# Kernel tuning notes

Measured on AMD Instinct MI355X. Metric: run time of the kernel, lower is better.

Reference implementation:

```python
import jax, jax.numpy as jnp
import numpy as np

EPS_LN = 1e-5
EPS_W = 1e-16
K = 3


def layernorm(x, gamma, beta):
    mu = x.mean(-1, keepdims=True)
    var = ((x - mu) ** 2).mean(-1, keepdims=True)
    return (x - mu) * jax.lax.rsqrt(var + EPS_LN) * gamma + beta


def knn_interp(xb, pos_x, pos_y, k=K):
    """Inverse-squared-distance kNN interpolation.
    xb: [B, Nx, C] source features; pos_x: [Nx, 3]; pos_y: [Ny, 3].
    Positions are identical across batch (torch code expands them), so the
    kNN search is done once and the gather is broadcast over batch.
    Returns [B, Ny, C]."""
    # squared distances via ||y||^2 + ||x||^2 - 2 y.x  -> [Ny, Nx]
    d2 = ((pos_y * pos_y).sum(-1)[:, None]
          + (pos_x * pos_x).sum(-1)[None, :]
          - 2.0 * pos_y @ pos_x.T)
    _, idx = jax.lax.top_k(-d2, k)                      # [Ny, k] nearest
    # exact squared distances for the selected neighbors (matches torch math)
    diff = pos_x[idx] - pos_y[:, None, :]               # [Ny, k, 3]
    w = 1.0 / jnp.clip((diff * diff).sum(-1), EPS_W)    # [Ny, k]
    xg = xb[:, idx, :]                                  # [B, Ny, k, C]
    num = (xg * w[None, :, :, None]).sum(2)             # [B, Ny, C]
    return num / w.sum(1)[None, :, None]


def setup_inputs() -> dict:
    key = jax.random.key(0)
    k1, k2, k3 = jax.random.split(key, 3)
    B, N_MESH, N_PIV, C = 4, 40000, 2000, 128
    return {
        "node_features": jax.random.normal(k1, (B * N_MESH, C), jnp.float32),
        "gamma": jnp.ones((C,), jnp.float32),
        "beta": jnp.zeros((C,), jnp.float32),
        "position_mesh": jax.random.uniform(k2, (N_MESH, 3), jnp.float32),
        "position_pivotal": jax.random.uniform(k3, (N_PIV, 3), jnp.float32),
        "batch_size": 4,
    }


def reference(node_features, gamma, beta, position_mesh, position_pivotal, batch_size):
    B = batch_size
    C = node_features.shape[-1]
    Nm = position_mesh.shape[0]
    # encode: PivotalNorm then mesh -> pivotal interpolation
    h = layernorm(node_features, gamma, beta)
    hb = h.reshape(B, Nm, C)
    piv = knn_interp(hb, position_mesh, position_pivotal, K)      # [B, Npiv, C]
    # decode: pivotal -> mesh interpolation
    mesh = knn_interp(piv, position_pivotal, position_mesh, K)    # [B, Nm, C]
    return mesh.reshape(B * Nm, C)
```

## Files before the change

kernel.cpp:

```cpp
#include <hip/hip_runtime.h>
#include <hip/hip_bf16.h>
#include <math.h>

#define EPS_LN 1e-5f
#define EPS_W  1e-16f

__device__ __forceinline__ float cvt(const __hip_bfloat16 v) { return __bfloat162float(v); }
__device__ __forceinline__ float cvt(const float v)          { return v; }

__device__ __forceinline__ void load8(const __hip_bfloat16* p, float* x) {
    union { uint4 v; __hip_bfloat16 h[8]; } t;
    t.v = *(const uint4*)p;
    #pragma unroll
    for (int i = 0; i < 8; ++i) x[i] = __bfloat162float(t.h[i]);
}
__device__ __forceinline__ void load8(const float* p, float* x) {
    float4 a = *(const float4*)p, b = *(const float4*)(p + 4);
    x[0]=a.x; x[1]=a.y; x[2]=a.z; x[3]=a.w; x[4]=b.x; x[5]=b.y; x[6]=b.z; x[7]=b.w;
}

__device__ __forceinline__ void ins3lex(float nd, int ni, float d[3], int ix[3]) {
    bool b2 = (nd < d[2]) || (nd == d[2] && ni < ix[2]);
    if (!b2) return;
    bool b1 = (nd < d[1]) || (nd == d[1] && ni < ix[1]);
    bool b0 = (nd < d[0]) || (nd == d[0] && ni < ix[0]);
    if (b0)      { d[2]=d[1]; ix[2]=ix[1]; d[1]=d[0]; ix[1]=ix[0]; d[0]=nd; ix[0]=ni; }
    else if (b1) { d[2]=d[1]; ix[2]=ix[1]; d[1]=nd; ix[1]=ni; }
    else         { d[2]=nd; ix[2]=ni; }
}

__global__ __launch_bounds__(256)
void stage_kernel(const void* pmesh, int Nm, const void* ppiv, int Np,
                  float4* __restrict__ mesh_s, float4* __restrict__ piv_s,
                  int* __restrict__ flag) {
    __shared__ int sbad;
    if (threadIdx.x == 0) sbad = 0;
    __syncthreads();
    {
        const __hip_bfloat16* pb = (const __hip_bfloat16*)ppiv;
        int bad = 0;
        for (int i = threadIdx.x; i < Np * 3; i += 256) {
            float v = __bfloat162float(pb[i]);
            if (!(v >= 0.0f && v <= 1.0f)) bad = 1;
        }
        if (bad) sbad = 1;
    }
    __syncthreads();
    const int isf32 = sbad;

    int gid = blockIdx.x * 256 + threadIdx.x;
    if (gid == 0) *flag = isf32;
    const int total = Nm + Np;
    if (gid >= total) return;
    const int isMesh = gid < Nm ? 1 : 0;
    const int idx = isMesh ? gid : gid - Nm;
    const void* src = isMesh ? pmesh : ppiv;
    float x, y, z;
    if (isf32) {
        const float* p = (const float*)src;
        x = p[idx*3+0]; y = p[idx*3+1]; z = p[idx*3+2];
    } else {
        const __hip_bfloat16* p = (const __hip_bfloat16*)src;
        x = cvt(p[idx*3+0]); y = cvt(p[idx*3+1]); z = cvt(p[idx*3+2]);
    }
    float4 o; o.x = x; o.y = y; o.z = z; o.w = x*x + y*y + z*z;
    (isMesh ? mesh_s : piv_s)[idx] = o;
}

__device__ __forceinline__ void scan_body(
        const float4* __restrict__ cand, int Nc,
        const float4* __restrict__ qry, int Nq,
        int blk, int nslice, int chunk,
        int* __restrict__ idx_out, float* __restrict__ wn_out,
        float2* __restrict__ partials,
        float sd[4][64][3], int si[4][64][3]) {
    const int tid   = threadIdx.x;
    const int lane  = tid & 63;
    const int wv    = __builtin_amdgcn_readfirstlane(tid >> 6);
    const int qg    = blk / nslice;
    const int slice = blk % nslice;
    const int q     = qg * 64 + lane;
    const int qc    = min(q, Nq - 1);

    const float4 qp = qry[qc];
    const float  qn = qp.w;

    float d0 = INFINITY, d1 = INFINITY, d2 = INFINITY;
    int   i0 = 0x7fffffff, i1 = 0x7fffffff, i2 = 0x7fffffff;

    const int jbeg = (slice * 4 + wv) * chunk;
    const int jend = min(jbeg + chunk, Nc);
    #pragma unroll 4
    for (int j = jbeg; j < jend; ++j) {
        const float4 cp = cand[j];
        float t   = qn + cp.w;
        float dot = qp.x*cp.x + qp.y*cp.y + qp.z*cp.z;
        float s   = t - 2.0f*dot;
        if (__any(s < d2)) {
            if (s < d2) {
                if (s < d1) {
                    d2 = d1; i2 = i1;
                    if (s < d0) { d1 = d0; i1 = i0; d0 = s; i0 = j; }
                    else        { d1 = s;  i1 = j; }
                } else { d2 = s; i2 = j; }
            }
        }
    }

    sd[wv][lane][0] = d0; sd[wv][lane][1] = d1; sd[wv][lane][2] = d2;
    si[wv][lane][0] = i0; si[wv][lane][1] = i1; si[wv][lane][2] = i2;
    __syncthreads();

    if (wv == 0) {
        float d[3]  = {d0, d1, d2};
        int   ix[3] = {i0, i1, i2};
        for (int w = 1; w < 4; ++w)
            for (int k = 0; k < 3; ++k)
                ins3lex(sd[w][lane][k], si[w][lane][k], d, ix);
        if (q < Nq) {
            if (nslice == 1) {
                float w_[3], ws = 0.f;
                for (int k = 0; k < 3; ++k) {
                    int ii = min(max(ix[k], 0), Nc - 1);
                    ix[k] = ii;
                    float4 cp = cand[ii];
                    float dx = cp.x - qp.x, dy = cp.y - qp.y, dz = cp.z - qp.z;
                    float dd = dx*dx + dy*dy + dz*dz;
                    w_[k] = 1.0f / fmaxf(dd, EPS_W);
                    ws += w_[k];
                }
                float inv = 1.0f / ws;
                for (int k = 0; k < 3; ++k) {
                    idx_out[q*3+k] = ix[k];
                    wn_out[q*3+k]  = w_[k] * inv;
                }
            } else {
                float2* p = partials + ((size_t)q * nslice + slice) * 3;
                for (int k = 0; k < 3; ++k) {
                    float2 e; e.x = d[k]; e.y = __int_as_float(ix[k]);
                    p[k] = e;
                }
            }
        }
    }
}

__global__ __launch_bounds__(256)
void knn_scan_fused(const float4* __restrict__ mesh_s, int Nm,
                    const float4* __restrict__ piv_s, int Np,
                    int nb1, int nsl1, int chk1, int nsl2, int chk2,
                    int* __restrict__ idx1, float* __restrict__ wn1,
                    float2* __restrict__ part1,
                    int* __restrict__ idx2, float* __restrict__ wn2,
                    float2* __restrict__ part2) {
    __shared__ float sd[4][64][3];
    __shared__ int   si[4][64][3];
    const int bid = blockIdx.x;
    if (bid < nb1) {
        scan_body(mesh_s, Nm, piv_s, Np, bid, nsl1, chk1,
                  idx1, wn1, part1, sd, si);
    } else {
        scan_body(piv_s, Np, mesh_s, Nm, bid - nb1, nsl2, chk2,
                  idx2, wn2, part2, sd, si);
    }
}

__device__ __forceinline__ void finalize_wave(
        const float2* __restrict__ partials, int nslice,
        const float4* __restrict__ cand, int Nc,
        const float4* __restrict__ qry, int q, int lane,
        int* __restrict__ idx_out, float* __restrict__ wn_out) {
    const int nent = nslice * 3;
    const float2* p = partials + (size_t)q * nent;

    float d[3]  = {INFINITY, INFINITY, INFINITY};
    int   ix[3] = {0x7fffffff, 0x7fffffff, 0x7fffffff};
    for (int e = lane; e < nent; e += 64)
        ins3lex(p[e].x, __float_as_int(p[e].y), d, ix);

    #pragma unroll
    for (int off = 32; off >= 1; off >>= 1) {
        float od[3]; int oix[3];
        #pragma unroll
        for (int k = 0; k < 3; ++k) {
            od[k]  = __shfl_xor(d[k],  off);
            oix[k] = __shfl_xor(ix[k], off);
        }
        #pragma unroll
        for (int k = 0; k < 3; ++k) ins3lex(od[k], oix[k], d, ix);
    }

    if (lane == 0) {
        const float4 qp = qry[q];
        float w_[3], ws = 0.f;
        for (int k = 0; k < 3; ++k) {
            int ii = min(max(ix[k], 0), Nc - 1);
            ix[k] = ii;
            float4 cp = cand[ii];
            float dx = cp.x - qp.x, dy = cp.y - qp.y, dz = cp.z - qp.z;
            float dd = dx*dx + dy*dy + dz*dz;
            w_[k] = 1.0f / fmaxf(dd, EPS_W);
            ws += w_[k];
        }
        float inv = 1.0f / ws;
        for (int k = 0; k < 3; ++k) {
            idx_out[q*3+k] = ix[k];
            wn_out[q*3+k]  = w_[k] * inv;
        }
    }
}

__global__ __launch_bounds__(256)
void knn_finalize_fused(const float2* __restrict__ part1, int nsl1,
                        const float4* __restrict__ mesh_s, int Nm,
                        const float4* __restrict__ piv_s, int Np,
                        const float2* __restrict__ part2, int nsl2,
                        int nq1, int nq2,
                        int* __restrict__ idx1, float* __restrict__ wn1,
                        int* __restrict__ idx2, float* __restrict__ wn2) {
    const int lane = threadIdx.x & 63;
    const int w = blockIdx.x * 4 + (threadIdx.x >> 6);
    if (w < nq1)
        finalize_wave(part1, nsl1, mesh_s, Nm, piv_s, w, lane, idx1, wn1);
    else if (w - nq1 < nq2)
        finalize_wave(part2, nsl2, piv_s, Np, mesh_s, w - nq1, lane, idx2, wn2);
}

template <typename T, typename S>
__device__ void interp_ln_wave4_body(const T* __restrict__ xfeat,
                                     const T* __restrict__ gamma,
                                     const T* __restrict__ beta,
                                     const int* __restrict__ idx,
                                     const float* __restrict__ wn,
                                     S* __restrict__ piv,
                                     int Nm, int Np, int C, int B) {
    const int tid  = threadIdx.x;
    const int lane = tid & 63;
    const int sub  = lane >> 4;
    const int l16  = lane & 15;
    const int row_id = (blockIdx.x * 4 + (tid >> 6)) * 4 + sub;
    if (row_id >= B * Np) return;
    const int b  = row_id / Np;
    const int j  = row_id - b * Np;
    const int c0 = l16 * 8;

    float g[8], be[8];
    load8(gamma + c0, g);
    load8(beta  + c0, be);

    const float invC = 1.0f / (float)C;
    float acc[8];
    #pragma unroll
    for (int t = 0; t < 8; ++t) acc[t] = 0.f;

    for (int k = 0; k < 3; ++k) {
        int row = idx[j*3+k];
        row = min(max(row, 0), Nm - 1);
        const T* xp = xfeat + ((size_t)b*Nm + row) * (size_t)C + c0;
        float x[8];
        load8(xp, x);
        float s = 0.f, s2 = 0.f;
        #pragma unroll
        for (int t = 0; t < 8; ++t) { s += x[t]; s2 += x[t]*x[t]; }
        #pragma unroll
        for (int off = 8; off >= 1; off >>= 1) {
            s  += __shfl_xor(s,  off);
            s2 += __shfl_xor(s2, off);
        }
        float mean = s * invC;
        float var  = s2 * invC - mean*mean;
        float rs   = rsqrtf(var + EPS_LN);
        float wk   = wn[j*3+k];
        #pragma unroll
        for (int t = 0; t < 8; ++t)
            acc[t] += wk * ((x[t] - mean)*rs*g[t] + be[t]);
    }

    S* pp = piv + ((size_t)b*Np + j) * (size_t)C + c0;
    if constexpr (sizeof(S) == 2) {
        union { uint4 v; S h[8]; } o;
        #pragma unroll
        for (int t = 0; t < 8; ++t) o.h[t] = __float2bfloat16(acc[t]);
        *(uint4*)pp = o.v;
    } else {
        float4 a, c;
        a.x = acc[0]; a.y = acc[1]; a.z = acc[2]; a.w = acc[3];
        c.x = acc[4]; c.y = acc[5]; c.z = acc[6]; c.w = acc[7];
        *(float4*)pp = a;
        *(float4*)(pp + 4) = c;
    }
}

__global__ __launch_bounds__(256)
void interp_ln_wave4_kernel(const void* xfeat, const void* gamma, const void* beta,
                            const int* idx, const float* wn, void* piv,
                            int Nm, int Np, int C, int B, const int* dtype_flag) {
    if (*dtype_flag)
        interp_ln_wave4_body<float, float>((const float*)xfeat, (const float*)gamma,
                                           (const float*)beta, idx, wn,
                                           (float*)piv, Nm, Np, C, B);
    else
        interp_ln_wave4_body<__hip_bfloat16, __hip_bfloat16>(
            (const __hip_bfloat16*)xfeat, (const __hip_bfloat16*)gamma,
            (const __hip_bfloat16*)beta, idx, wn,
            (__hip_bfloat16*)piv, Nm, Np, C, B);
}

template <typename T, typename S>
__device__ void interp_ln_body(const T* __restrict__ xfeat,
                               const T* __restrict__ gamma,
                               const T* __restrict__ beta,
                               const int* __restrict__ idx,
                               const float* __restrict__ wn,
                               S* __restrict__ piv, int Nm, int Np, int C) {
    const int j   = blockIdx.x % Np;
    const int b   = blockIdx.x / Np;
    const int c   = threadIdx.x;
    const int wid = c >> 6;
    const int nw  = C >> 6;

    const float g  = cvt(gamma[c]);
    const float be = cvt(beta[c]);

    __shared__ float red[8];
    float acc = 0.f;
    const float invC = 1.0f / (float)C;

    for (int k = 0; k < 3; ++k) {
        int row = idx[j*3+k];
        row = min(max(row, 0), Nm - 1);
        const T* xp = xfeat + ((size_t)b*Nm + row) * (size_t)C;
        float x = cvt(xp[c]);
        float s = x, s2 = x*x;
        for (int off = 32; off > 0; off >>= 1) {
            s  += __shfl_down(s,  off);
            s2 += __shfl_down(s2, off);
        }
        if ((c & 63) == 0) { red[wid] = s; red[4+wid] = s2; }
        __syncthreads();
        float sum = 0.f, sum2 = 0.f;
        for (int w = 0; w < nw; ++w) { sum += red[w]; sum2 += red[4+w]; }
        float mean = sum * invC;
        float var  = sum2 * invC - mean*mean;
        float rs   = rsqrtf(var + EPS_LN);
        acc += wn[j*3+k] * ((x - mean)*rs*g + be);
        __syncthreads();
    }
    S ov; if constexpr (sizeof(S) == 2) ov = __float2bfloat16(acc); else ov = acc;
    piv[((size_t)b*Np + j) * (size_t)C + c] = ov;
}

__global__ __launch_bounds__(128)
void interp_ln_kernel(const void* xfeat, const void* gamma, const void* beta,
                      const int* idx, const float* wn, void* piv,
                      int Nm, int Np, int C, const int* dtype_flag) {
    if (*dtype_flag)
        interp_ln_body<float, float>((const float*)xfeat, (const float*)gamma,
                                     (const float*)beta, idx, wn,
                                     (float*)piv, Nm, Np, C);
    else
        interp_ln_body<__hip_bfloat16, __hip_bfloat16>(
            (const __hip_bfloat16*)xfeat, (const __hip_bfloat16*)gamma,
            (const __hip_bfloat16*)beta, idx, wn,
            (__hip_bfloat16*)piv, Nm, Np, C);
}

__global__ __launch_bounds__(256)
void gather_out8_kernel(const void* __restrict__ pivv,
                        const int* __restrict__ idx, const float* __restrict__ wn,
                        void* __restrict__ out, int Nm, int Np, int C, int B,
                        int total, const int* __restrict__ dtype_flag) {
    int gid = blockIdx.x * 256 + threadIdx.x;
    if (gid >= total) return;
    const int C8 = C >> 3;
    const int c8 = gid % C8;
    const int i  = gid / C8;
    int jj0 = min(max(idx[i*3+0], 0), Np - 1);
    int jj1 = min(max(idx[i*3+1], 0), Np - 1);
    int jj2 = min(max(idx[i*3+2], 0), Np - 1);
    const float w0 = wn[i*3+0], w1 = wn[i*3+1], w2 = wn[i*3+2];
    const int cb = c8 * 8;

    if (*dtype_flag) {
        const float* pv = (const float*)pivv;
        float* po = (float*)out;
        for (int b = 0; b < B; ++b) {
            const float* pb = pv + (size_t)b * Np * C;
            const float* r0 = pb + (size_t)jj0 * C + cb;
            const float* r1 = pb + (size_t)jj1 * C + cb;
            const float* r2 = pb + (size_t)jj2 * C + cb;
            float* qo = po + ((size_t)b*Nm + i) * (size_t)C + cb;
            #pragma unroll
            for (int h = 0; h < 2; ++h) {
                float4 v0 = *(const float4*)(r0 + h*4);
                float4 v1 = *(const float4*)(r1 + h*4);
                float4 v2 = *(const float4*)(r2 + h*4);
                float4 o;
                o.x = w0*v0.x + w1*v1.x + w2*v2.x;
                o.y = w0*v0.y + w1*v1.y + w2*v2.y;
                o.z = w0*v0.z + w1*v1.z + w2*v2.z;
                o.w = w0*v0.w + w1*v1.w + w2*v2.w;
                *(float4*)(qo + h*4) = o;
            }
        }
    } else {
        const __hip_bfloat16* pv = (const __hip_bfloat16*)pivv;
        __hip_bfloat16* po = (__hip_bfloat16*)out;
        for (int b = 0; b < B; ++b) {
            const __hip_bfloat16* pb = pv + (size_t)b * Np * C;
            union { uint4 v; __hip_bfloat16 h[8]; } u0, u1, u2, o;
            u0.v = *(const uint4*)(pb + (size_t)jj0 * C + cb);
            u1.v = *(const uint4*)(pb + (size_t)jj1 * C + cb);
            u2.v = *(const uint4*)(pb + (size_t)jj2 * C + cb);
            #pragma unroll
            for (int t = 0; t < 8; ++t) {
                float a = w0*cvt(u0.h[t]) + w1*cvt(u1.h[t]) + w2*cvt(u2.h[t]);
                o.h[t] = __float2bfloat16(a);
            }
            *(uint4*)(po + ((size_t)b*Nm + i) * (size_t)C + cb) = o.v;
        }
    }
}

__global__ __launch_bounds__(256)
void gather_out_kernel(const void* __restrict__ pivv,
                       const int* __restrict__ idx, const float* __restrict__ wn,
                       void* __restrict__ out, int Nm, int Np, int C4,
                       int total4, const int* __restrict__ dtype_flag) {
    int gid = blockIdx.x * 256 + threadIdx.x;
    if (gid >= total4) return;
    int c4 = gid % C4;
    int r  = gid / C4;
    int i  = r % Nm;
    int b  = r / Nm;
    const int C = C4 * 4;
    int jj0 = min(max(idx[i*3+0], 0), Np - 1);
    int jj1 = min(max(idx[i*3+1], 0), Np - 1);
    int jj2 = min(max(idx[i*3+2], 0), Np - 1);
    float w0 = wn[i*3+0], w1 = wn[i*3+1], w2 = wn[i*3+2];

    if (*dtype_flag) {
        const float* pbase = (const float*)pivv + (size_t)b * Np * C;
        float4 v0 = *(const float4*)(pbase + (size_t)jj0 * C + c4*4);
        float4 v1 = *(const float4*)(pbase + (size_t)jj1 * C + c4*4);
        float4 v2 = *(const float4*)(pbase + (size_t)jj2 * C + c4*4);
        float4 o;
        o.x = w0*v0.x + w1*v1.x + w2*v2.x;
        o.y = w0*v0.y + w1*v1.y + w2*v2.y;
        o.z = w0*v0.z + w1*v1.z + w2*v2.z;
        o.w = w0*v0.w + w1*v1.w + w2*v2.w;
        *(((float4*)out) + gid) = o;
    } else {
        const __hip_bfloat16* pbase = (const __hip_bfloat16*)pivv + (size_t)b * Np * C;
        union { __hip_bfloat16 h[4]; uint2 v; } u0, u1, u2, o;
        u0.v = *(const uint2*)(pbase + (size_t)jj0 * C + c4*4);
        u1.v = *(const uint2*)(pbase + (size_t)jj1 * C + c4*4);
        u2.v = *(const uint2*)(pbase + (size_t)jj2 * C + c4*4);
        #pragma unroll
        for (int t = 0; t < 4; ++t) {
            float a = w0*cvt(u0.h[t]) + w1*cvt(u1.h[t]) + w2*cvt(u2.h[t]);
            o.h[t] = __float2bfloat16(a);
        }
        *(((uint2*)out) + gid) = o.v;
    }
}

__global__ void zero_words_kernel(unsigned* out, long long nwords) {
    long long i = (long long)blockIdx.x * 256 + threadIdx.x;
    if (i < nwords) out[i] = 0u;
}

extern "C" void kernel_launch(void* const* d_in, const int* in_sizes, int n_in,
                              void* d_out, int out_size, void* d_ws, size_t ws_size,
                              hipStream_t stream) {
    const int C  = in_sizes[1];
    const int Nm = in_sizes[3] / 3;
    const int Np = in_sizes[4] / 3;
    const int B  = in_sizes[0] / (Nm * C);

    const int nqg1 = (Np + 63) / 64;
    const int nqg2 = (Nm + 63) / 64;

    auto plan = [](int nqg, int Nc, int& nsl, int& chk) {
        nsl = (2048 + nqg - 1) / nqg;
        int maxsl = (Nc + 127) / 128;
        if (nsl > maxsl) nsl = maxsl;
        if (nsl < 1) nsl = 1;
        chk = (Nc + nsl*4 - 1) / (nsl*4);
    };
    int nsl1, chk1, nsl2, chk2;
    plan(nqg1, Nm, nsl1, chk1);
    plan(nqg2, Np, nsl2, chk2);

    size_t off = 0;
    size_t flag_o = 0, meshs_o = 0, pivs_o = 0, piv_o = 0;
    size_t i1_o = 0, w1_o = 0, i2_o = 0, w2_o = 0, p1_o = 0, p2_o = 0;
    auto layout = [&](int s1, int s2) {
        off = 0;
        auto carve = [&](size_t bytes) {
            size_t p = off;
            off += (bytes + 255) & ~(size_t)255;
            return p;
        };
        flag_o  = carve(256);
        meshs_o = carve((size_t)Nm * sizeof(float4));
        pivs_o  = carve((size_t)Np * sizeof(float4));
        piv_o   = carve((size_t)B * Np * C * sizeof(float));
        i1_o    = carve((size_t)Np * 3 * sizeof(int));
        w1_o    = carve((size_t)Np * 3 * sizeof(float));
        i2_o    = carve((size_t)Nm * 3 * sizeof(int));
        w2_o    = carve((size_t)Nm * 3 * sizeof(float));
        p1_o    = carve((size_t)Np * s1 * 3 * sizeof(float2));
        p2_o    = carve((size_t)Nm * s2 * 3 * sizeof(float2));
    };
    layout(nsl1, nsl2);
    if (off > ws_size) {
        nsl1 = 16; chk1 = (Nm + nsl1*4 - 1) / (nsl1*4);
        nsl2 = 1;  chk2 = (Np + nsl2*4 - 1) / (nsl2*4);
        layout(nsl1, nsl2);
    }
    if (off > ws_size) {
        long long nwords = (long long)out_size / 2;
        zero_words_kernel<<<(int)((nwords + 255) / 256), 256, 0, stream>>>(
            (unsigned*)d_out, nwords);
        return;
    }

    char* base = (char*)d_ws;
    int*    flag   = (int*)   (base + flag_o);
    float4* mesh_s = (float4*)(base + meshs_o);
    float4* piv_s  = (float4*)(base + pivs_o);
    void*   piv    = (void*)  (base + piv_o);
    int*    idx1   = (int*)   (base + i1_o);
    float*  wn1    = (float*) (base + w1_o);
    int*    idx2   = (int*)   (base + i2_o);
    float*  wn2    = (float*) (base + w2_o);
    float2* part1  = (float2*)(base + p1_o);
    float2* part2  = (float2*)(base + p2_o);

    stage_kernel<<<(Nm + Np + 255) / 256, 256, 0, stream>>>(
        d_in[3], Nm, d_in[4], Np, mesh_s, piv_s, flag);

    const int nb1 = nqg1 * nsl1;
    const int nb2 = nqg2 * nsl2;
    knn_scan_fused<<<nb1 + nb2, 256, 0, stream>>>(
        mesh_s, Nm, piv_s, Np, nb1, nsl1, chk1, nsl2, chk2,
        idx1, wn1, part1, idx2, wn2, part2);

    const int nq1 = (nsl1 > 1) ? Np : 0;
    const int nq2 = (nsl2 > 1) ? Nm : 0;
    if (nq1 + nq2 > 0)
        knn_finalize_fused<<<(nq1 + nq2 + 3) / 4, 256, 0, stream>>>(
            part1, nsl1, mesh_s, Nm, piv_s, Np, part2, nsl2,
            nq1, nq2, idx1, wn1, idx2, wn2);

    if (C == 128) {
        const int nrow = B * Np;
        interp_ln_wave4_kernel<<<(nrow + 15) / 16, 256, 0, stream>>>(
            d_in[0], d_in[1], d_in[2], idx1, wn1, piv, Nm, Np, C, B, flag);
    } else {
        interp_ln_kernel<<<B * Np, C, 0, stream>>>(d_in[0], d_in[1], d_in[2],
                                                   idx1, wn1, piv, Nm, Np, C, flag);
    }

    if ((C & 7) == 0) {
        const int total = Nm * (C >> 3);
        gather_out8_kernel<<<(total + 255) / 256, 256, 0, stream>>>(
            piv, idx2, wn2, d_out, Nm, Np, C, B, total, flag);
    } else {
        const int C4 = C / 4;
        const int total4 = B * Nm * C4;
        gather_out_kernel<<<(total4 + 255) / 256, 256, 0, stream>>>(
            piv, idx2, wn2, d_out, Nm, Np, C4, total4, flag);
    }
}
```

Measured before the change: 265.0 us.

## Use uniform grid spatial binning for mesh-to-pivotal kNN search

Replaces the brute-force scan of all 40k mesh points per pivotal query with a uniform 3D grid: points are counted per cell, prefix-summed, and scattered into cell order. Each wave then searches growing shells of cells around its query and stops once the shell distance bound exceeds the current third-nearest distance. A brute-force fallback runs when mesh positions fall outside the unit cube. It also drops the wave-level __any guard in the remaining brute-force scan. The cost is four extra small launches (zero, count, single-block scan, scatter), atomics, and divergent shell loops, in exchange for far fewer distance evaluations.

```diff
diff --git a/kernel.cpp b/kernel.cpp
--- a/kernel.cpp
+++ b/kernel.cpp
@@ -4,6 +4,8 @@
 
 #define EPS_LN 1e-5f
 #define EPS_W  1e-16f
+#define SLACK_KNN 1e-4f
+#define IMAX 0x7fffffff
 
 __device__ __forceinline__ float cvt(const __hip_bfloat16 v) { return __bfloat162float(v); }
 __device__ __forceinline__ float cvt(const float v)          { return v; }
@@ -29,10 +31,24 @@
     else         { d[2]=nd; ix[2]=ni; }
 }
 
+__device__ __forceinline__ void wave_merge3(float d[3], int ix[3]) {
+    #pragma unroll
+    for (int off = 32; off >= 1; off >>= 1) {
+        float od[3]; int oix[3];
+        #pragma unroll
+        for (int k = 0; k < 3; ++k) {
+            od[k]  = __shfl_xor(d[k],  off);
+            oix[k] = __shfl_xor(ix[k], off);
+        }
+        #pragma unroll
+        for (int k = 0; k < 3; ++k) ins3lex(od[k], oix[k], d, ix);
+    }
+}
+
 __global__ __launch_bounds__(256)
 void stage_kernel(const void* pmesh, int Nm, const void* ppiv, int Np,
                   float4* __restrict__ mesh_s, float4* __restrict__ piv_s,
-                  int* __restrict__ flag) {
+                  int* __restrict__ flag, int* __restrict__ counts, int G1) {
     __shared__ int sbad;
     if (threadIdx.x == 0) sbad = 0;
     __syncthreads();
@@ -49,7 +65,7 @@
     const int isf32 = sbad;
 
     int gid = blockIdx.x * 256 + threadIdx.x;
-    if (gid == 0) *flag = isf32;
+    if (gid == 0) flag[0] = isf32;
     const int total = Nm + Np;
     if (gid >= total) return;
     const int isMesh = gid < Nm ? 1 : 0;
@@ -65,6 +81,63 @@
     }
     float4 o; o.x = x; o.y = y; o.z = z; o.w = x*x + y*y + z*z;
     (isMesh ? mesh_s : piv_s)[idx] = o;
+
+    if (isMesh) {
+        int cx = min(max((int)(x * (float)G1), 0), G1 - 1);
+        int cy = min(max((int)(y * (float)G1), 0), G1 - 1);
+        int cz = min(max((int)(z * (float)G1), 0), G1 - 1);
+        atomicAdd(&counts[(cz * G1 + cy) * G1 + cx], 1);
+        bool ok = (x >= 0.f && x <= 1.f && y >= 0.f && y <= 1.f &&
+                   z >= 0.f && z <= 1.f);
+        if (!ok) atomicOr(&flag[1], 1);
+    }
+}
+
+__global__ __launch_bounds__(256)
+void scan_kernel(const int* __restrict__ counts, int n,
+                 int* __restrict__ starts, int* __restrict__ cursors) {
+    __shared__ int carry;
+    __shared__ int wsum[4];
+    if (threadIdx.x == 0) carry = 0;
+    __syncthreads();
+    const int lane = threadIdx.x & 63;
+    const int wv   = threadIdx.x >> 6;
+    for (int base = 0; base < n; base += 256) {
+        int i = base + threadIdx.x;
+        int v = (i < n) ? counts[i] : 0;
+        int s = v;
+        #pragma unroll
+        for (int off = 1; off < 64; off <<= 1) {
+            int t = __shfl_up(s, off);
+            if (lane >= off) s += t;
+        }
+        if (lane == 63) wsum[wv] = s;
+        __syncthreads();
+        int woff = 0;
+        for (int w = 0; w < wv; ++w) woff += wsum[w];
+        int excl = carry + woff + (s - v);
+        if (i < n) { starts[i] = excl; cursors[i] = excl; }
+        __syncthreads();
+        if (threadIdx.x == 255) carry += woff + s;
+        __syncthreads();
+    }
+    if (threadIdx.x == 0) starts[n] = carry;
+}
+
+__global__ __launch_bounds__(256)
+void scatter_kernel(const float4* __restrict__ mesh_s, int Nm, int G1,
+                    int* __restrict__ cursors,
+                    float4* __restrict__ cellPts, int* __restrict__ cellIdx) {
+    int gid = blockIdx.x * 256 + threadIdx.x;
+    if (gid >= Nm) return;
+    float4 p = mesh_s[gid];
+    int cx = min(max((int)(p.x * (float)G1), 0), G1 - 1);
+    int cy = min(max((int)(p.y * (float)G1), 0), G1 - 1);
+    int cz = min(max((int)(p.z * (float)G1), 0), G1 - 1);
+    int c = (cz * G1 + cy) * G1 + cx;
+    int pos = atomicAdd(&cursors[c], 1);
+    cellPts[pos] = p;
+    cellIdx[pos] = gid;
 }
 
 __device__ __forceinline__ void scan_body(
@@ -86,7 +159,7 @@
     const float  qn = qp.w;
 
     float d0 = INFINITY, d1 = INFINITY, d2 = INFINITY;
-    int   i0 = 0x7fffffff, i1 = 0x7fffffff, i2 = 0x7fffffff;
+    int   i0 = IMAX, i1 = IMAX, i2 = IMAX;
 
     const int jbeg = (slice * 4 + wv) * chunk;
     const int jend = min(jbeg + chunk, Nc);
@@ -96,14 +169,12 @@
         float t   = qn + cp.w;
         float dot = qp.x*cp.x + qp.y*cp.y + qp.z*cp.z;
         float s   = t - 2.0f*dot;
-        if (__any(s < d2)) {
-            if (s < d2) {
-                if (s < d1) {
-                    d2 = d1; i2 = i1;
-                    if (s < d0) { d1 = d0; i1 = i0; d0 = s; i0 = j; }
-                    else        { d1 = s;  i1 = j; }
-                } else { d2 = s; i2 = j; }
-            }
+        if (s < d2) {
+            if (s < d1) {
+                d2 = d1; i2 = i1;
+                if (s < d0) { d1 = d0; i1 = i0; d0 = s; i0 = j; }
+                else        { d1 = s;  i1 = j; }
+            } else { d2 = s; i2 = j; }
         }
     }
 
@@ -146,49 +217,160 @@
 }
 
 __global__ __launch_bounds__(256)
-void knn_scan_fused(const float4* __restrict__ mesh_s, int Nm,
-                    const float4* __restrict__ piv_s, int Np,
-                    int nb1, int nsl1, int chk1, int nsl2, int chk2,
-                    int* __restrict__ idx1, float* __restrict__ wn1,
-                    float2* __restrict__ part1,
-                    int* __restrict__ idx2, float* __restrict__ wn2,
-                    float2* __restrict__ part2) {
+void knn_fused(const float4* __restrict__ mesh_s, int Nm,
+               const float4* __restrict__ piv_s, int Np,
+               const int* __restrict__ starts,
+               const float4* __restrict__ cellPts,
+               const int* __restrict__ cellIdx,
+               int G1, int nbW, int nsl2, int chk2,
+               int* __restrict__ idx1, float* __restrict__ wn1,
+               int* __restrict__ idx2, float* __restrict__ wn2,
+               float2* __restrict__ part2,
+               const int* __restrict__ flags) {
     __shared__ float sd[4][64][3];
     __shared__ int   si[4][64][3];
     const int bid = blockIdx.x;
-    if (bid < nb1) {
-        scan_body(mesh_s, Nm, piv_s, Np, bid, nsl1, chk1,
-                  idx1, wn1, part1, sd, si);
+
+    if (bid >= nbW) {
+        scan_body(piv_s, Np, mesh_s, Nm, bid - nbW, nsl2, chk2,
+                  idx2, wn2, part2, sd, si);
+        return;
+    }
+
+    const int lane = threadIdx.x & 63;
+    const int wv   = threadIdx.x >> 6;
+    const int q    = bid * 4 + wv;
+    if (q >= Np) return;
+
+    const float4 qp = piv_s[q];
+    const float  qn = qp.w;
+    float d[3]  = {INFINITY, INFINITY, INFINITY};
+    int   ix[3] = {IMAX, IMAX, IMAX};
+
+    if (!flags[1]) {
+        const float Gf = (float)G1;
+        const float h  = 1.0f / Gf;
+        int cx = min(max((int)(qp.x * Gf), 0), G1 - 1);
+        int cy = min(max((int)(qp.y * Gf), 0), G1 - 1);
+        int cz = min(max((int)(qp.z * Gf), 0), G1 - 1);
+        cx = __builtin_amdgcn_readfirstlane(cx);
+        cy = __builtin_amdgcn_readfirstlane(cy);
+        cz = __builtin_amdgcn_readfirstlane(cz);
+        float fx0 = qp.x - (float)cx * h,  fx1 = (float)(cx+1) * h - qp.x;
+        float fy0 = qp.y - (float)cy * h,  fy1 = (float)(cy+1) * h - qp.y;
+        float fz0 = qp.z - (float)cz * h,  fz1 = (float)(cz+1) * h - qp.z;
+        float fmin = fminf(fminf(fminf(fx0, fx1), fminf(fy0, fy1)),
+                           fminf(fz0, fz1));
+
+        for (int r = 0; r <= G1; ++r) {
+            if (r >= 2) {
+                float md[3] = {d[0], d[1], d[2]};
+                int   mi[3] = {ix[0], ix[1], ix[2]};
+                wave_merge3(md, mi);
+                if (mi[2] != IMAX) {
+                    float bound = (float)(r - 1) * h + fmin;
+                    if (bound > 0.f && bound * bound - SLACK_KNN > md[2])
+                        break;
+                }
+            }
+            for (int dz = -r; dz <= r; ++dz) {
+                int z = cz + dz; if (z < 0 || z >= G1) continue;
+                int adz = dz < 0 ? -dz : dz;
+                for (int dy = -r; dy <= r; ++dy) {
+                    int y = cy + dy; if (y < 0 || y >= G1) continue;
+                    int ady = dy < 0 ? -dy : dy;
+                    int rowbase = (z * G1 + y) * G1;
+                    int pb, pe;
+                    if (max(adz, ady) == r || r == 0) {
+                        int x0 = max(cx - r, 0), x1 = min(cx + r, G1 - 1);
+                        pb = starts[rowbase + x0];
+                        pe = starts[rowbase + x1 + 1];
+                        for (int b0 = pb; b0 < pe; b0 += 64) {
+                            int p = b0 + lane;
+                            if (p < pe) {
+                                float4 cp = cellPts[p];
+                                float t   = qn + cp.w;
+                                float dot = qp.x*cp.x + qp.y*cp.y + qp.z*cp.z;
+                                float s   = t - 2.0f*dot;
+                                ins3lex(s, cellIdx[p], d, ix);
+                            }
+                        }
+                    } else {
+                        #pragma unroll
+                        for (int side = 0; side < 2; ++side) {
+                            int x = side ? cx + r : cx - r;
+                            if (x < 0 || x >= G1) continue;
+                            pb = starts[rowbase + x];
+                            pe = starts[rowbase + x + 1];
+                            for (int b0 = pb; b0 < pe; b0 += 64) {
+                                int p = b0 + lane;
+                                if (p < pe) {
+                                    float4 cp = cellPts[p];
+                                    float t   = qn + cp.w;
+                                    float dot = qp.x*cp.x + qp.y*cp.y + qp.z*cp.z;
+                                    float s   = t - 2.0f*dot;
+                                    ins3lex(s, cellIdx[p], d, ix);
+                                }
+                            }
+                        }
+                    }
+                }
+            }
+        }
     } else {
-        scan_body(piv_s, Np, mesh_s, Nm, bid - nb1, nsl2, chk2,
-                  idx2, wn2, part2, sd, si);
-    }
-}
-
-__device__ __forceinline__ void finalize_wave(
-        const float2* __restrict__ partials, int nslice,
-        const float4* __restrict__ cand, int Nc,
-        const float4* __restrict__ qry, int q, int lane,
-        int* __restrict__ idx_out, float* __restrict__ wn_out) {
+        for (int b0 = 0; b0 < Nm; b0 += 64) {
+            int p = b0 + lane;
+            if (p < Nm) {
+                float4 cp = mesh_s[p];
+                float t   = qn + cp.w;
+                float dot = qp.x*cp.x + qp.y*cp.y + qp.z*cp.z;
+                float s   = t - 2.0f*dot;
+                ins3lex(s, p, d, ix);
+            }
+        }
+    }
+
+    wave_merge3(d, ix);
+
+    if (lane == 0) {
+        float w_[3], ws = 0.f;
+        #pragma unroll
+        for (int k = 0; k < 3; ++k) {
+            int ii = min(max(ix[k], 0), Nm - 1);
+            ix[k] = ii;
+            float4 cp = mesh_s[ii];
+            float dx = cp.x - qp.x, dy = cp.y - qp.y, dz = cp.z - qp.z;
+            float dd = dx*dx + dy*dy + dz*dz;
+            w_[k] = 1.0f / fmaxf(dd, EPS_W);
+            ws += w_[k];
+        }
+        float inv = 1.0f / ws;
+        #pragma unroll
+        for (int k = 0; k < 3; ++k) {
+            idx1[q*3+k] = ix[k];
+            wn1[q*3+k]  = w_[k] * inv;
+        }
+    }
+}
+
+__global__ __launch_bounds__(256)
+void knn_finalize_kernel(const float2* __restrict__ partials, int nslice,
+                         const float4* __restrict__ cand, int Nc,
+                         const float4* __restrict__ qry, int Nq,
+                         int* __restrict__ idx_out, float* __restrict__ wn_out) {
+    const int lane = threadIdx.x & 63;
+    const int q    = blockIdx.x * 4 + (threadIdx.x >> 6);
+    if (q >= Nq) return;
+
     const int nent = nslice * 3;
     const float2* p = partials + (size_t)q * nent;
 
     float d[3]  = {INFINITY, INFINITY, INFINITY};
-    int   ix[3] = {0x7fffffff, 0x7fffffff, 0x7fffffff};
+    int   ix[3] = {IMAX, IMAX, IMAX};
     for (int e = lane; e < nent; e += 64)
         ins3lex(p[e].x, __float_as_int(p[e].y), d, ix);
 
-    #pragma unroll
-    for (int off = 32; off >= 1; off >>= 1) {
-        float od[3]; int oix[3];
-        #pragma unroll
-        for (int k = 0; k < 3; ++k) {
-            od[k]  = __shfl_xor(d[k],  off);
-            oix[k] = __shfl_xor(ix[k], off);
-        }
-        #pragma unroll
-        for (int k = 0; k < 3; ++k) ins3lex(od[k], oix[k], d, ix);
-    }
+    wave_merge3(d, ix);
 
     if (lane == 0) {
         const float4 qp = qry[q];
@@ -208,22 +390,6 @@
             wn_out[q*3+k]  = w_[k] * inv;
         }
     }
-}
-
-__global__ __launch_bounds__(256)
-void knn_finalize_fused(const float2* __restrict__ part1, int nsl1,
-                        const float4* __restrict__ mesh_s, int Nm,
-                        const float4* __restrict__ piv_s, int Np,
-                        const float2* __restrict__ part2, int nsl2,
-                        int nq1, int nq2,
-                        int* __restrict__ idx1, float* __restrict__ wn1,
-                        int* __restrict__ idx2, float* __restrict__ wn2) {
-    const int lane = threadIdx.x & 63;
-    const int w = blockIdx.x * 4 + (threadIdx.x >> 6);
-    if (w < nq1)
-        finalize_wave(part1, nsl1, mesh_s, Nm, piv_s, w, lane, idx1, wn1);
-    else if (w - nq1 < nq2)
-        finalize_wave(part2, nsl2, piv_s, Np, mesh_s, w - nq1, lane, idx2, wn2);
 }
 
 template <typename T, typename S>
@@ -478,47 +644,41 @@
     const int Np = in_sizes[4] / 3;
     const int B  = in_sizes[0] / (Nm * C);
 
-    const int nqg1 = (Np + 63) / 64;
+    int G1 = (int)cbrtf((float)Nm / 4.0f);
+    if (G1 < 1) G1 = 1;
+    if (G1 > 48) G1 = 48;
+    const int C1 = G1 * G1 * G1;
+
     const int nqg2 = (Nm + 63) / 64;
-
-    auto plan = [](int nqg, int Nc, int& nsl, int& chk) {
-        nsl = (2048 + nqg - 1) / nqg;
-        int maxsl = (Nc + 127) / 128;
-        if (nsl > maxsl) nsl = maxsl;
-        if (nsl < 1) nsl = 1;
-        chk = (Nc + nsl*4 - 1) / (nsl*4);
+    int nsl2 = (2048 + nqg2 - 1) / nqg2;
+    {
+        int maxsl = (Np + 127) / 128;
+        if (nsl2 > maxsl) nsl2 = maxsl;
+        if (nsl2 < 1) nsl2 = 1;
+    }
+    const int chk2 = (Np + nsl2*4 - 1) / (nsl2*4);
+
+    size_t off = 0;
+    auto carve = [&](size_t bytes) {
+        size_t p = off;
+        off += (bytes + 255) & ~(size_t)255;
+        return p;
     };
-    int nsl1, chk1, nsl2, chk2;
-    plan(nqg1, Nm, nsl1, chk1);
-    plan(nqg2, Np, nsl2, chk2);
-
-    size_t off = 0;
-    size_t flag_o = 0, meshs_o = 0, pivs_o = 0, piv_o = 0;
-    size_t i1_o = 0, w1_o = 0, i2_o = 0, w2_o = 0, p1_o = 0, p2_o = 0;
-    auto layout = [&](int s1, int s2) {
-        off = 0;
-        auto carve = [&](size_t bytes) {
-            size_t p = off;
-            off += (bytes + 255) & ~(size_t)255;
-            return p;
-        };
-        flag_o  = carve(256);
-        meshs_o = carve((size_t)Nm * sizeof(float4));
-        pivs_o  = carve((size_t)Np * sizeof(float4));
-        piv_o   = carve((size_t)B * Np * C * sizeof(float));
-        i1_o    = carve((size_t)Np * 3 * sizeof(int));
-        w1_o    = carve((size_t)Np * 3 * sizeof(float));
-        i2_o    = carve((size_t)Nm * 3 * sizeof(int));
-        w2_o    = carve((size_t)Nm * 3 * sizeof(float));
-        p1_o    = carve((size_t)Np * s1 * 3 * sizeof(float2));
-        p2_o    = carve((size_t)Nm * s2 * 3 * sizeof(float2));
-    };
-    layout(nsl1, nsl2);
-    if (off > ws_size) {
-        nsl1 = 16; chk1 = (Nm + nsl1*4 - 1) / (nsl1*4);
-        nsl2 = 1;  chk2 = (Np + nsl2*4 - 1) / (nsl2*4);
-        layout(nsl1, nsl2);
-    }
+    const size_t flag_o   = carve(256);
+    const size_t counts_o = carve((size_t)C1 * 4);
+    const size_t starts_o = carve((size_t)(C1 + 1) * 4);
+    const size_t curs_o   = carve((size_t)C1 * 4);
+    const size_t cpts_o   = carve((size_t)Nm * sizeof(float4));
+    const size_t cidx_o   = carve((size_t)Nm * 4);
+    const size_t meshs_o  = carve((size_t)Nm * sizeof(float4));
+    const size_t pivs_o   = carve((size_t)Np * sizeof(float4));
+    const size_t piv_o    = carve((size_t)B * Np * C * sizeof(float));
+    const size_t i1_o     = carve((size_t)Np * 3 * 4);
+    const size_t w1_o     = carve((size_t)Np * 3 * 4);
+    const size_t i2_o     = carve((size_t)Nm * 3 * 4);
+    const size_t w2_o     = carve((size_t)Nm * 3 * 4);
+    const size_t p2_o     = carve((size_t)Nm * nsl2 * 3 * sizeof(float2));
+
     if (off > ws_size) {
         long long nwords = (long long)out_size / 2;
         zero_words_kernel<<<(int)((nwords + 255) / 256), 256, 0, stream>>>(
@@ -528,6 +688,11 @@
 
     char* base = (char*)d_ws;
     int*    flag   = (int*)   (base + flag_o);
+    int*    counts = (int*)   (base + counts_o);
+    int*    starts = (int*)   (base + starts_o);
+    int*    curs   = (int*)   (base + curs_o);
+    float4* cpts   = (float4*)(base + cpts_o);
+    int*    cidx   = (int*)   (base + cidx_o);
     float4* mesh_s = (float4*)(base + meshs_o);
     float4* piv_s  = (float4*)(base + pivs_o);
     void*   piv    = (void*)  (base + piv_o);
@@ -535,24 +700,31 @@
     float*  wn1    = (float*) (base + w1_o);
     int*    idx2   = (int*)   (base + i2_o);
     float*  wn2    = (float*) (base + w2_o);
-    float2* part1  = (float2*)(base + p1_o);
     float2* part2  = (float2*)(base + p2_o);
 
+    {
+        long long nwords = 64 + (long long)C1;
+        zero_words_kernel<<<(int)((nwords + 255) / 256), 256, 0, stream>>>(
+            (unsigned*)flag, nwords);
+    }
+
     stage_kernel<<<(Nm + Np + 255) / 256, 256, 0, stream>>>(
-        d_in[3], Nm, d_in[4], Np, mesh_s, piv_s, flag);
-
-    const int nb1 = nqg1 * nsl1;
+        d_in[3], Nm, d_in[4], Np, mesh_s, piv_s, flag, counts, G1);
+
+    scan_kernel<<<1, 256, 0, stream>>>(counts, C1, starts, curs);
+
+    scatter_kernel<<<(Nm + 255) / 256, 256, 0, stream>>>(
+        mesh_s, Nm, G1, curs, cpts, cidx);
+
+    const int nbW = (Np + 3) / 4;
     const int nb2 = nqg2 * nsl2;
-    knn_scan_fused<<<nb1 + nb2, 256, 0, stream>>>(
-        mesh_s, Nm, piv_s, Np, nb1, nsl1, chk1, nsl2, chk2,
-        idx1, wn1, part1, idx2, wn2, part2);
-
-    const int nq1 = (nsl1 > 1) ? Np : 0;
-    const int nq2 = (nsl2 > 1) ? Nm : 0;
-    if (nq1 + nq2 > 0)
-        knn_finalize_fused<<<(nq1 + nq2 + 3) / 4, 256, 0, stream>>>(
-            part1, nsl1, mesh_s, Nm, piv_s, Np, part2, nsl2,
-            nq1, nq2, idx1, wn1, idx2, wn2);
+    knn_fused<<<nbW + nb2, 256, 0, stream>>>(
+        mesh_s, Nm, piv_s, Np, starts, cpts, cidx,
+        G1, nbW, nsl2, chk2, idx1, wn1, idx2, wn2, part2, flag);
+
+    if (nsl2 > 1)
+        knn_finalize_kernel<<<(Nm + 3) / 4, 256, 0, stream>>>(
+            part2, nsl2, piv_s, Np, mesh_s, Nm, idx2, wn2);
 
     if (C == 128) {
         const int nrow = B * Np;
```

Measured after the change: 275.0 us. +3.8%, slower.
